# Kernel tuning notes

Measured on AMD Instinct MI355X. Metric: run time of the kernel, lower is better.

The kernel has to match this reference:

```python
import jax, jax.numpy as jnp
import numpy as np

N_NODES = 50000
N_EDGES = 800000
D = 128


def sage_conv(x, src, dst, w_nbr, w_root, b, n_nodes):
    # mean aggregation of neighbor features: messages flow src (j) -> dst (i)
    msg_sum = jax.ops.segment_sum(x[src], dst, num_segments=n_nodes)  # [N, D]
    deg = jax.ops.segment_sum(jnp.ones((src.shape[0],), x.dtype), dst,
                              num_segments=n_nodes)
    mean = msg_sum / jnp.maximum(deg, 1.0)[:, None]
    # PyG SAGEConv: lin_l(aggr) + lin_r(x); bias lives in lin_l
    return mean @ w_nbr + x @ w_root + b


def setup_inputs() -> dict:
    key = jax.random.key(0)
    ks = jax.random.split(key, 16)
    s = 1.0 / np.sqrt(D)
    inp = {
        "x": jax.random.normal(ks[0], (N_NODES, D), jnp.float32),
        "edge_index": jax.random.randint(ks[1], (2, N_EDGES), 0, N_NODES,
                                         dtype=jnp.int64),
    }
    for l in range(3):
        inp[f"w_nbr{l}"] = jax.random.normal(ks[2 + 3 * l], (D, D), jnp.float32) * s
        inp[f"w_root{l}"] = jax.random.normal(ks[3 + 3 * l], (D, D), jnp.float32) * s
        inp[f"b{l}"] = jnp.zeros((D,), jnp.float32)
    inp["w_cls"] = jax.random.normal(ks[12], (D, 1), jnp.float32) * s
    inp["b_cls"] = jnp.zeros((1,), jnp.float32)
    return inp


def reference(x, edge_index, w_nbr0, w_root0, b0, w_nbr1, w_root1, b1,
              w_nbr2, w_root2, b2, w_cls, b_cls):
    src, dst = edge_index[0], edge_index[1]
    n = x.shape[0]
    layers = [(w_nbr0, w_root0, b0), (w_nbr1, w_root1, b1), (w_nbr2, w_root2, b2)]
    h = x
    for i, (wn, wr, b) in enumerate(layers):
        h = sage_conv(h, src, dst, wn, wr, b, n)
        if i < len(layers) - 1:
            h = jax.nn.relu(h)  # dropout is identity in eval mode
    return (h @ w_cls + b_cls).squeeze(-1)  # [N]
```

## Files before the change

### kernel.cpp

```cpp
#include <hip/hip_runtime.h>

#define N_NODES 50000
#define N_EDGES 800000
#define D 128
#define NGROUPS 3125
#define NBUK 256
#define NPB 196
#define EPB 4096
#define NBLK 196
#define LTOT (NBUK * NBLK)
#define NSCB 49

typedef __attribute__((ext_vector_type(8))) short short8;
typedef __attribute__((ext_vector_type(4))) float f32x4;

__device__ __forceinline__ float bits2f(unsigned int u) {
    union { unsigned int u; float f; } c; c.u = u; return c.f;
}
__device__ __forceinline__ unsigned short f2b(float f) {
    union { float f; unsigned int u; } c; c.f = f;
    unsigned int r = c.u + 0x7fffu + ((c.u >> 16) & 1u);
    return (unsigned short)(r >> 16);
}


__global__ __launch_bounds__(256) void k_big(
    const int* __restrict__ dst, int* __restrict__ cnt,
    const float* __restrict__ x,
    const float* __restrict__ wn0, const float* __restrict__ wr0,
    const float* __restrict__ wn1, const float* __restrict__ wr1,
    const float* __restrict__ wn2, const float* __restrict__ wr2,
    const float* __restrict__ b2, const float* __restrict__ wc,
    const float* __restrict__ bc,
    unsigned short* __restrict__ f0, unsigned short* __restrict__ f1,
    unsigned short* __restrict__ f2, unsigned short* __restrict__ Bp,
    float* __restrict__ uvc) {
    __shared__ int lc[NBUK];
    int b = blockIdx.x;
    int tid = threadIdx.x;
    if (b < NBLK) {
        lc[tid] = 0;
        __syncthreads();
        #pragma unroll
        for (int k = 0; k < 16; ++k) {
            int e = b * EPB + k * 256 + tid;
            if (e < N_EDGES) atomicAdd(&lc[dst[e] / NPB], 1);
        }
        __syncthreads();
        cnt[b * NBUK + tid] = lc[tid];
    } else if (b < 6446) {
        int i = (b - NBLK) * 256 + tid;
        float4 v = reinterpret_cast<const float4*>(x)[i];
        ushort4 o;
        o.x = f2b(v.x); o.y = f2b(v.y); o.z = f2b(v.z); o.w = f2b(v.w);
        reinterpret_cast<ushort4*>(f0)[i] = o;
    } else if (b < 6478) {
        int t = (b - 6446) * 256 + tid;
        int layer = t >> 12;
        int rem = t & 4095;
        int kstep = rem >> 9;
        int cf = (rem >> 6) & 7;
        int lane = t & 63;
        const float* W = (kstep < 4) ? (layer ? wn1 : wn0) : (layer ? wr1 : wr0);
        int kb = kstep * 32 + (lane >> 4) * 8;
        int colv = cf * 16 + (lane & 15);
        int koff = (kstep < 4) ? kb : kb - 128;
        unsigned short* dstp = Bp + (((layer * 64 + kstep * 8 + cf) * 64 + lane) << 3);
        #pragma unroll
        for (int i = 0; i < 8; ++i) dstp[i] = f2b(W[(koff + i) * D + colv]);
    } else if (b == 6478) {
        if (tid < D) {
            f0[(size_t)N_NODES * D + tid] = 0;
            f1[(size_t)N_NODES * D + tid] = 0;
            f2[(size_t)N_NODES * D + tid] = 0;
        }
    } else {
        if (tid < 128) {
            float su = 0.f;
            for (int m = 0; m < 128; ++m) su += wn2[tid * D + m] * wc[m];
            uvc[tid] = su;
        } else {
            int k = tid - 128;
            float sv = 0.f;
            for (int m = 0; m < 128; ++m) sv += wr2[k * D + m] * wc[m];
            uvc[128 + k] = sv;
        }
        if (tid == 0) {
            float sc0 = 0.f;
            for (int m = 0; m < 128; ++m) sc0 += b2[m] * wc[m];
            uvc[256] = sc0 + bc[0];
        }
    }
}


__global__ void k_scanA(const int* __restrict__ cnt, int* __restrict__ sc,
                        int* __restrict__ bsumA) {
    __shared__ int wsum[16];
    int tid = threadIdx.x;
    int lane = tid & 63, wid = tid >> 6;
    int L = blockIdx.x * 1024 + tid;
    int v = 0;
    if (L < LTOT) {
        int bkt = L / NBLK;
        int j = L - bkt * NBLK;
        v = cnt[j * NBUK + bkt];
    }
    int s = v;
    #pragma unroll
    for (int off = 1; off < 64; off <<= 1) {
        int t = __shfl_up(s, off, 64);
        if (lane >= off) s += t;
    }
    if (lane == 63) wsum[wid] = s;
    __syncthreads();
    if (tid < 64) {
        int wv = (tid < 16) ? wsum[tid] : 0;
        int t = wv;
        #pragma unroll
        for (int off = 1; off < 16; off <<= 1) {
            int u = __shfl_up(t, off, 64);
            if (tid >= off) t += u;
        }
        if (tid < 16) wsum[tid] = t - wv;
    }
    __syncthreads();
    int excl = s - v + wsum[wid];
    if (L < LTOT) sc[L] = excl;
    if (tid == 1023) bsumA[blockIdx.x] = excl + v;
}


__global__ __launch_bounds__(256) void k_scatter(
    const int* __restrict__ src, const int* __restrict__ dst,
    const int* __restrict__ sc, const int* __restrict__ bsumA,
    int2* __restrict__ epair) {
    __shared__ int sb[64];
    __shared__ int cursor[NBUK];
    int tid = threadIdx.x, j = blockIdx.x;
    if (tid < 64) sb[tid] = (tid < NSCB) ? bsumA[tid] : 0;
    __syncthreads();
    for (int off = 1; off < 64; off <<= 1) {
        int t = (tid < 64 && tid >= off) ? sb[tid - off] : 0;
        __syncthreads();
        if (tid < 64) sb[tid] += t;
        __syncthreads();
    }
    int L = tid * NBLK + j;
    int idx = L >> 10;
    cursor[tid] = sc[L] + (idx ? sb[idx - 1] : 0);
    __syncthreads();
    #pragma unroll
    for (int k = 0; k < 16; ++k) {
        int e = j * EPB + k * 256 + tid;
        if (e < N_EDGES) {
            int d = dst[e];
            int p = atomicAdd(&cursor[d / NPB], 1);
            epair[p] = make_int2(d, src[e]);
        }
    }
}


__global__ __launch_bounds__(256) void k_bucket(
    const int* __restrict__ sc, const int* __restrict__ bsumA,
    const int2* __restrict__ epair,
    int* __restrict__ rs, int* __restrict__ col) {
    __shared__ int sb[64];
    __shared__ int lcnt[NPB];
    __shared__ int s2[256];
    __shared__ int cur[NPB];
    int tid = threadIdx.x, b = blockIdx.x;
    if (tid < 64) sb[tid] = (tid < NSCB) ? bsumA[tid] : 0;
    __syncthreads();
    for (int off = 1; off < 64; off <<= 1) {
        int t = (tid < 64 && tid >= off) ? sb[tid - off] : 0;
        __syncthreads();
        if (tid < 64) sb[tid] += t;
        __syncthreads();
    }
    int L0 = b * NBLK;
    int i0 = L0 >> 10;
    int gstart = sc[L0] + (i0 ? sb[i0 - 1] : 0);
    int bend = N_EDGES;
    if (b + 1 < NBUK) {
        int L1 = (b + 1) * NBLK;
        int i1 = L1 >> 10;
        bend = sc[L1] + (i1 ? sb[i1 - 1] : 0);
    }
    if (tid < NPB) lcnt[tid] = 0;
    __syncthreads();
    for (int e = gstart + tid; e < bend; e += 256)
        atomicAdd(&lcnt[epair[e].x - b * NPB], 1);
    __syncthreads();
    int v = (tid < NPB) ? lcnt[tid] : 0;
    s2[tid] = v;
    __syncthreads();
    for (int off = 1; off < 256; off <<= 1) {
        int t = (tid >= off) ? s2[tid - off] : 0;
        __syncthreads();
        s2[tid] += t;
        __syncthreads();
    }
    int excl = s2[tid] - v;
    int node = b * NPB + tid;
    if (tid < NPB) {
        if (node <= N_NODES) rs[node] = gstart + excl;
        cur[tid] = gstart + excl;
    }
    __syncthreads();
    for (int e = gstart + tid; e < bend; e += 256) {
        int2 p2 = epair[e];
        int p = atomicAdd(&cur[p2.x - b * NPB], 1);
        col[p] = p2.y;
    }
    if (b == NBUK - 1 && tid == 0) rs[N_NODES] = N_EDGES;
}


#define ACCUM(v)                                                      \
    acc0 += bits2f((v).x << 16); acc1 += bits2f((v).x & 0xffff0000u); \
    acc2 += bits2f((v).y << 16); acc3 += bits2f((v).y & 0xffff0000u); \
    acc4 += bits2f((v).z << 16); acc5 += bits2f((v).z & 0xffff0000u); \
    acc6 += bits2f((v).w << 16); acc7 += bits2f((v).w & 0xffff0000u);

__global__ __launch_bounds__(256) void k_agg2(const unsigned short* __restrict__ h,
                                              const int* __restrict__ rs,
                                              const int* __restrict__ col,
                                              unsigned short* __restrict__ mean) {
    const int lane = threadIdx.x & 63;
    const int node = blockIdx.x * 4 + (threadIdx.x >> 6);
    if (node >= N_NODES) return;
    const int j0 = rs[node], j1 = rs[node + 1];
    const int deg = j1 - j0;
    const int q = lane >> 4;
    const int d8 = (lane & 15) * 8;

    int myc = (j0 + lane < j1) ? col[j0 + lane] : N_NODES;
    const int nfull = deg < 64 ? deg : 64;
    const int nb = (nfull + 15) >> 4;

    float acc0 = 0.f, acc1 = 0.f, acc2 = 0.f, acc3 = 0.f;
    float acc4 = 0.f, acc5 = 0.f, acc6 = 0.f, acc7 = 0.f;

    for (int i = 0; i < nb; ++i) {
        int t = (i << 4) + q;
        int c0 = __shfl(myc, t, 64);
        int c1 = __shfl(myc, t + 4, 64);
        int c2 = __shfl(myc, t + 8, 64);
        int c3 = __shfl(myc, t + 12, 64);
        uint4 v0 = *(const uint4*)(h + (size_t)c0 * D + d8);
        uint4 v1 = *(const uint4*)(h + (size_t)c1 * D + d8);
        uint4 v2 = *(const uint4*)(h + (size_t)c2 * D + d8);
        uint4 v3 = *(const uint4*)(h + (size_t)c3 * D + d8);
        ACCUM(v0); ACCUM(v1); ACCUM(v2); ACCUM(v3);
    }
    for (int j = j0 + 64 + q; j < j1; j += 4) {
        int c = col[j];
        uint4 v = *(const uint4*)(h + (size_t)c * D + d8);
        ACCUM(v);
    }

    acc0 += __shfl_xor(acc0, 16, 64); acc0 += __shfl_xor(acc0, 32, 64);
    acc1 += __shfl_xor(acc1, 16, 64); acc1 += __shfl_xor(acc1, 32, 64);
    acc2 += __shfl_xor(acc2, 16, 64); acc2 += __shfl_xor(acc2, 32, 64);
    acc3 += __shfl_xor(acc3, 16, 64); acc3 += __shfl_xor(acc3, 32, 64);
    acc4 += __shfl_xor(acc4, 16, 64); acc4 += __shfl_xor(acc4, 32, 64);
    acc5 += __shfl_xor(acc5, 16, 64); acc5 += __shfl_xor(acc5, 32, 64);
    acc6 += __shfl_xor(acc6, 16, 64); acc6 += __shfl_xor(acc6, 32, 64);
    acc7 += __shfl_xor(acc7, 16, 64); acc7 += __shfl_xor(acc7, 32, 64);

    if (lane < 16) {
        float s = 1.0f / (float)(deg > 0 ? deg : 1);
        uint4 o;
        o.x = (unsigned int)f2b(acc0 * s) | ((unsigned int)f2b(acc1 * s) << 16);
        o.y = (unsigned int)f2b(acc2 * s) | ((unsigned int)f2b(acc3 * s) << 16);
        o.z = (unsigned int)f2b(acc4 * s) | ((unsigned int)f2b(acc5 * s) << 16);
        o.w = (unsigned int)f2b(acc6 * s) | ((unsigned int)f2b(acc7 * s) << 16);
        *reinterpret_cast<uint4*>(mean + (size_t)node * D + d8) = o;
    }
}


__global__ __launch_bounds__(256) void k_gemm(
    const unsigned short* __restrict__ Amean, const unsigned short* __restrict__ Ah,
    const unsigned short* __restrict__ Bp, const float* __restrict__ bias,
    unsigned short* __restrict__ outh) {
    int lane = threadIdx.x & 63;
    int w = blockIdx.x * 4 + (threadIdx.x >> 6);
    int g0 = w * 2;
    if (g0 >= NGROUPS) return;
    int g1ok = (g0 + 1 < NGROUPS);
    int hl = lane & 15;
    int klane = (lane >> 4) * 8;
    int arow0 = g0 * 16 + hl;
    int arow1 = g0 * 16 + 16 + hl;
    if (arow1 > N_NODES) arow1 = N_NODES;

    f32x4 acc0[8], acc1[8];
    #pragma unroll
    for (int i = 0; i < 8; ++i) { acc0[i] = (f32x4)0.0f; acc1[i] = (f32x4)0.0f; }

    const short8* bpv = reinterpret_cast<const short8*>(Bp);
    #pragma unroll
    for (int kstep = 0; kstep < 8; ++kstep) {
        const unsigned short* Asrc = (kstep < 4) ? Amean : Ah;
        int kk = (kstep & 3) * 32 + klane;
        short8 a0 = *reinterpret_cast<const short8*>(Asrc + (size_t)arow0 * D + kk);
        short8 a1 = *reinterpret_cast<const short8*>(Asrc + (size_t)arow1 * D + kk);
        #pragma unroll
        for (int cf = 0; cf < 8; ++cf) {
            short8 b = bpv[(kstep * 8 + cf) * 64 + lane];
            acc0[cf] = __builtin_amdgcn_mfma_f32_16x16x32_bf16(a0, b, acc0[cf], 0, 0, 0);
            acc1[cf] = __builtin_amdgcn_mfma_f32_16x16x32_bf16(a1, b, acc1[cf], 0, 0, 0);
        }
    }

    int rbase0 = g0 * 16 + (lane >> 4) * 4;
    #pragma unroll
    for (int cf = 0; cf < 8; ++cf) {
        int bcol = cf * 16 + hl;
        float bv = bias[bcol];
        #pragma unroll
        for (int i = 0; i < 4; ++i) {
            float v = fmaxf(acc0[cf][i] + bv, 0.f);
            outh[(size_t)(rbase0 + i) * D + bcol] = f2b(v);
            if (g1ok) {
                float v1 = fmaxf(acc1[cf][i] + bv, 0.f);
                outh[(size_t)(rbase0 + 16 + i) * D + bcol] = f2b(v1);
            }
        }
    }
}


__global__ __launch_bounds__(256) void k_gemm_dot(
    const unsigned short* __restrict__ Amean, const unsigned short* __restrict__ Ah,
    const unsigned short* __restrict__ Bp, const float* __restrict__ bias,
    const float* __restrict__ uvc, float* __restrict__ s, float* __restrict__ t) {
    int lane = threadIdx.x & 63;
    int w = blockIdx.x * 4 + (threadIdx.x >> 6);
    int g0 = w * 2;
    if (g0 >= NGROUPS) return;
    int g1ok = (g0 + 1 < NGROUPS);
    int hl = lane & 15;
    int klane = (lane >> 4) * 8;
    int arow0 = g0 * 16 + hl;
    int arow1 = g0 * 16 + 16 + hl;
    if (arow1 > N_NODES) arow1 = N_NODES;

    f32x4 acc0[8], acc1[8];
    #pragma unroll
    for (int i = 0; i < 8; ++i) { acc0[i] = (f32x4)0.0f; acc1[i] = (f32x4)0.0f; }

    const short8* bpv = reinterpret_cast<const short8*>(Bp);
    #pragma unroll
    for (int kstep = 0; kstep < 8; ++kstep) {
        const unsigned short* Asrc = (kstep < 4) ? Amean : Ah;
        int kk = (kstep & 3) * 32 + klane;
        short8 a0 = *reinterpret_cast<const short8*>(Asrc + (size_t)arow0 * D + kk);
        short8 a1 = *reinterpret_cast<const short8*>(Asrc + (size_t)arow1 * D + kk);
        #pragma unroll
        for (int cf = 0; cf < 8; ++cf) {
            short8 b = bpv[(kstep * 8 + cf) * 64 + lane];
            acc0[cf] = __builtin_amdgcn_mfma_f32_16x16x32_bf16(a0, b, acc0[cf], 0, 0, 0);
            acc1[cf] = __builtin_amdgcn_mfma_f32_16x16x32_bf16(a1, b, acc1[cf], 0, 0, 0);
        }
    }

    float ps0[4] = {0.f, 0.f, 0.f, 0.f}, pt0[4] = {0.f, 0.f, 0.f, 0.f};
    float ps1[4] = {0.f, 0.f, 0.f, 0.f}, pt1[4] = {0.f, 0.f, 0.f, 0.f};
    #pragma unroll
    for (int cf = 0; cf < 8; ++cf) {
        int bcol = cf * 16 + hl;
        float bv = bias[bcol];
        float uu = uvc[bcol];
        float vv = uvc[128 + bcol];
        #pragma unroll
        for (int i = 0; i < 4; ++i) {
            float v = fmaxf(acc0[cf][i] + bv, 0.f);
            ps0[i] += v * uu;
            pt0[i] += v * vv;
            float v1 = fmaxf(acc1[cf][i] + bv, 0.f);
            ps1[i] += v1 * uu;
            pt1[i] += v1 * vv;
        }
    }
    #pragma unroll
    for (int m = 1; m < 16; m <<= 1) {
        #pragma unroll
        for (int i = 0; i < 4; ++i) {
            ps0[i] += __shfl_xor(ps0[i], m, 64);
            pt0[i] += __shfl_xor(pt0[i], m, 64);
            ps1[i] += __shfl_xor(ps1[i], m, 64);
            pt1[i] += __shfl_xor(pt1[i], m, 64);
        }
    }
    if (hl == 0) {
        int rbase0 = g0 * 16 + (lane >> 4) * 4;
        #pragma unroll
        for (int i = 0; i < 4; ++i) {
            s[rbase0 + i] = ps0[i];
            t[rbase0 + i] = pt0[i];
            if (g1ok) {
                s[rbase0 + 16 + i] = ps1[i];
                t[rbase0 + 16 + i] = pt1[i];
            }
        }
    }
}

__global__ __launch_bounds__(256) void k_sagg2(const float* __restrict__ s,
                                               const float* __restrict__ t,
                                               const float* __restrict__ uvc,
                                               const int* __restrict__ rs,
                                               const int* __restrict__ col,
                                               float* __restrict__ out) {
    const int lane = threadIdx.x & 63;
    const int hl = lane & 15;
    const int node = blockIdx.x * 16 + (threadIdx.x >> 6) * 4 + (lane >> 4);
    const int j0 = rs[node], j1 = rs[node + 1];
    float sm = 0.f;
    for (int j = j0 + hl; j < j1; j += 16) sm += s[col[j]];
    #pragma unroll
    for (int m = 1; m < 16; m <<= 1) sm += __shfl_xor(sm, m, 64);
    if (hl == 0) {
        int deg = j1 - j0;
        out[node] = sm / (float)(deg > 0 ? deg : 1) + t[node] + uvc[256];
    }
}


extern "C" void kernel_launch(void* const* d_in, const int* in_sizes, int n_in,
                              void* d_out, int out_size, void* d_ws,
                              size_t ws_size, hipStream_t stream) {
    const float* x = (const float*)d_in[0];
    const int* ei = (const int*)d_in[1];
    const int* src = ei;
    const int* dst = ei + N_EDGES;
    const float* wn[3] = {(const float*)d_in[2], (const float*)d_in[5],
                          (const float*)d_in[8]};
    const float* wr[3] = {(const float*)d_in[3], (const float*)d_in[6],
                          (const float*)d_in[9]};
    const float* bs[3] = {(const float*)d_in[4], (const float*)d_in[7],
                          (const float*)d_in[10]};
    const float* wc = (const float*)d_in[11];
    const float* bc = (const float*)d_in[12];
    float* out = (float*)d_out;

    char* ws = (char*)d_ws;
    size_t off = 0;
    auto alloc = [&](size_t bytes) -> void* {
        void* p = (void*)(ws + off);
        off += (bytes + 255) & ~(size_t)255;
        return p;
    };
    const size_t frows = (size_t)(N_NODES + 1) * D;
    int* cnt = (int*)alloc((size_t)LTOT * 4);
    int* sc = (int*)alloc((size_t)LTOT * 4);
    int* bsumA = (int*)alloc(64 * 4);
    int2* epair = (int2*)alloc((size_t)N_EDGES * 8);
    int* rs = (int*)alloc((N_NODES + 1) * 4);
    int* col = (int*)alloc(N_EDGES * 4);
    unsigned short* f0 = (unsigned short*)alloc(frows * 2);
    unsigned short* f1 = (unsigned short*)alloc(frows * 2);
    unsigned short* f2 = (unsigned short*)alloc(frows * 2);
    unsigned short* Bp = (unsigned short*)alloc(2 * 256 * 128 * 2);
    float* uvc = (float*)alloc(260 * 4);
    float* sbuf = (float*)alloc(N_NODES * 4);
    float* tbuf = (float*)alloc(N_NODES * 4);


    k_big<<<6480, 256, 0, stream>>>(dst, cnt, x, wn[0], wr[0], wn[1], wr[1],
                                    wn[2], wr[2], bs[2], wc, bc,
                                    f0, f1, f2, Bp, uvc);
    k_scanA<<<NSCB, 1024, 0, stream>>>(cnt, sc, bsumA);
    k_scatter<<<NBLK, 256, 0, stream>>>(src, dst, sc, bsumA, epair);
    k_bucket<<<NBUK, 256, 0, stream>>>(sc, bsumA, epair, rs, col);

    const int agg_grid = (N_NODES + 3) / 4;
    const int gemm_grid = ((NGROUPS + 1) / 2 + 3) / 4;
    unsigned short* Bp0 = Bp;
    unsigned short* Bp1 = Bp + 256 * 128;

    k_agg2<<<agg_grid, 256, 0, stream>>>(f0, rs, col, f1);
    k_gemm<<<gemm_grid, 256, 0, stream>>>(f1, f0, Bp0, bs[0], f2);
    k_agg2<<<agg_grid, 256, 0, stream>>>(f2, rs, col, f0);
    k_gemm_dot<<<gemm_grid, 256, 0, stream>>>(f0, f2, Bp1, bs[1], uvc, sbuf,
                                              tbuf);
    k_sagg2<<<NGROUPS, 256, 0, stream>>>(sbuf, tbuf, uvc, rs, col, out);
}
```

Measured before the change: 135.0 us.

## Remove scan kernel by recomputing bucket offsets redundantly in scatter and bucket kernels

Drops the separate k_scanA launch and its sc/bsumA buffers. Each k_scatter and k_bucket block now reads the whole 196x256 count matrix, sums per-bucket totals and does a 256-wide exclusive scan in shared memory to derive its cursors and ranges. This saves one kernel launch and its dependency gap in exchange for redundant reads of about 200KB of counts per block, served mostly from cache.

```diff
diff --git a/kernel.cpp b/kernel.cpp
--- a/kernel.cpp
+++ b/kernel.cpp
@@ -9,7 +9,6 @@
 #define EPB 4096
 #define NBLK 196
 #define LTOT (NBUK * NBLK)
-#define NSCB 49
 
 typedef __attribute__((ext_vector_type(8))) short short8;
 typedef __attribute__((ext_vector_type(4))) float f32x4;
@@ -21,6 +20,25 @@
     union { float f; unsigned int u; } c; c.f = f;
     unsigned int r = c.u + 0x7fffu + ((c.u >> 16) & 1u);
     return (unsigned short)(r >> 16);
+}
+
+__device__ __forceinline__ int excl_scan256(int v, int* wsum) {
+    int lane = threadIdx.x & 63, wid = threadIdx.x >> 6;
+    int s = v;
+    #pragma unroll
+    for (int off = 1; off < 64; off <<= 1) {
+        int t = __shfl_up(s, off, 64);
+        if (lane >= off) s += t;
+    }
+    if (lane == 63) wsum[wid] = s;
+    __syncthreads();
+    if (threadIdx.x == 0) {
+        int r = 0;
+        #pragma unroll
+        for (int k = 0; k < 4; ++k) { int t = wsum[k]; wsum[k] = r; r += t; }
+    }
+    __syncthreads();
+    return s - v + wsum[wid];
 }
 
 
@@ -94,61 +112,20 @@
 }
 
 
-__global__ void k_scanA(const int* __restrict__ cnt, int* __restrict__ sc,
-                        int* __restrict__ bsumA) {
-    __shared__ int wsum[16];
-    int tid = threadIdx.x;
-    int lane = tid & 63, wid = tid >> 6;
-    int L = blockIdx.x * 1024 + tid;
-    int v = 0;
-    if (L < LTOT) {
-        int bkt = L / NBLK;
-        int j = L - bkt * NBLK;
-        v = cnt[j * NBUK + bkt];
-    }
-    int s = v;
-    #pragma unroll
-    for (int off = 1; off < 64; off <<= 1) {
-        int t = __shfl_up(s, off, 64);
-        if (lane >= off) s += t;
-    }
-    if (lane == 63) wsum[wid] = s;
-    __syncthreads();
-    if (tid < 64) {
-        int wv = (tid < 16) ? wsum[tid] : 0;
-        int t = wv;
-        #pragma unroll
-        for (int off = 1; off < 16; off <<= 1) {
-            int u = __shfl_up(t, off, 64);
-            if (tid >= off) t += u;
-        }
-        if (tid < 16) wsum[tid] = t - wv;
-    }
-    __syncthreads();
-    int excl = s - v + wsum[wid];
-    if (L < LTOT) sc[L] = excl;
-    if (tid == 1023) bsumA[blockIdx.x] = excl + v;
-}
-
-
 __global__ __launch_bounds__(256) void k_scatter(
     const int* __restrict__ src, const int* __restrict__ dst,
-    const int* __restrict__ sc, const int* __restrict__ bsumA,
-    int2* __restrict__ epair) {
-    __shared__ int sb[64];
+    const int* __restrict__ cnt, int2* __restrict__ epair) {
+    __shared__ int wsum[4];
     __shared__ int cursor[NBUK];
     int tid = threadIdx.x, j = blockIdx.x;
-    if (tid < 64) sb[tid] = (tid < NSCB) ? bsumA[tid] : 0;
-    __syncthreads();
-    for (int off = 1; off < 64; off <<= 1) {
-        int t = (tid < 64 && tid >= off) ? sb[tid - off] : 0;
-        __syncthreads();
-        if (tid < 64) sb[tid] += t;
-        __syncthreads();
-    }
-    int L = tid * NBLK + j;
-    int idx = L >> 10;
-    cursor[tid] = sc[L] + (idx ? sb[idx - 1] : 0);
+    int tot = 0, part = 0;
+    for (int jp = 0; jp < NBLK; ++jp) {
+        int c = cnt[jp * NBUK + tid];
+        tot += c;
+        part += (jp < j) ? c : 0;
+    }
+    int colstart = excl_scan256(tot, wsum);
+    cursor[tid] = colstart + part;
     __syncthreads();
     #pragma unroll
     for (int k = 0; k < 16; ++k) {
@@ -163,31 +140,20 @@
 
 
 __global__ __launch_bounds__(256) void k_bucket(
-    const int* __restrict__ sc, const int* __restrict__ bsumA,
-    const int2* __restrict__ epair,
+    const int* __restrict__ cnt, const int2* __restrict__ epair,
     int* __restrict__ rs, int* __restrict__ col) {
-    __shared__ int sb[64];
+    __shared__ int wsum[4];
+    __shared__ int gse[2];
     __shared__ int lcnt[NPB];
     __shared__ int s2[256];
     __shared__ int cur[NPB];
     int tid = threadIdx.x, b = blockIdx.x;
-    if (tid < 64) sb[tid] = (tid < NSCB) ? bsumA[tid] : 0;
-    __syncthreads();
-    for (int off = 1; off < 64; off <<= 1) {
-        int t = (tid < 64 && tid >= off) ? sb[tid - off] : 0;
-        __syncthreads();
-        if (tid < 64) sb[tid] += t;
-        __syncthreads();
-    }
-    int L0 = b * NBLK;
-    int i0 = L0 >> 10;
-    int gstart = sc[L0] + (i0 ? sb[i0 - 1] : 0);
-    int bend = N_EDGES;
-    if (b + 1 < NBUK) {
-        int L1 = (b + 1) * NBLK;
-        int i1 = L1 >> 10;
-        bend = sc[L1] + (i1 ? sb[i1 - 1] : 0);
-    }
+    int tot = 0;
+    for (int jp = 0; jp < NBLK; ++jp) tot += cnt[jp * NBUK + tid];
+    int colstart = excl_scan256(tot, wsum);
+    if (tid == b) { gse[0] = colstart; gse[1] = colstart + tot; }
+    __syncthreads();
+    int gstart = gse[0], bend = gse[1];
     if (tid < NPB) lcnt[tid] = 0;
     __syncthreads();
     for (int e = gstart + tid; e < bend; e += 256)
@@ -457,8 +423,6 @@
     };
     const size_t frows = (size_t)(N_NODES + 1) * D;
     int* cnt = (int*)alloc((size_t)LTOT * 4);
-    int* sc = (int*)alloc((size_t)LTOT * 4);
-    int* bsumA = (int*)alloc(64 * 4);
     int2* epair = (int2*)alloc((size_t)N_EDGES * 8);
     int* rs = (int*)alloc((N_NODES + 1) * 4);
     int* col = (int*)alloc(N_EDGES * 4);
@@ -474,9 +438,8 @@
     k_big<<<6480, 256, 0, stream>>>(dst, cnt, x, wn[0], wr[0], wn[1], wr[1],
                                     wn[2], wr[2], bs[2], wc, bc,
                                     f0, f1, f2, Bp, uvc);
-    k_scanA<<<NSCB, 1024, 0, stream>>>(cnt, sc, bsumA);
-    k_scatter<<<NBLK, 256, 0, stream>>>(src, dst, sc, bsumA, epair);
-    k_bucket<<<NBUK, 256, 0, stream>>>(sc, bsumA, epair, rs, col);
+    k_scatter<<<NBLK, 256, 0, stream>>>(src, dst, cnt, epair);
+    k_bucket<<<NBUK, 256, 0, stream>>>(cnt, epair, rs, col);
 
     const int agg_grid = (N_NODES + 3) / 4;
     const int gemm_grid = ((NGROUPS + 1) / 2 + 3) / 4;
```

New measurement: 141.4 us. 1.05x slower.
